# Optimization experiments

Measured on AMD Instinct MI355X. Metric: run time of the kernel, lower is better.

The kernel has to match this reference:

```python
import jax, jax.numpy as jnp
import numpy as np

N_NODES = 100000


def gcn_conv(x, W, b, src, dst, n):
    # PyG GCNConv: add self-loops, symmetric deg^-1/2 normalization,
    # transform then gather/scatter-add aggregate.
    loop = jnp.arange(n, dtype=src.dtype)
    s = jnp.concatenate([src, loop])
    d = jnp.concatenate([dst, loop])
    deg = jax.ops.segment_sum(jnp.ones_like(d, dtype=x.dtype), d, num_segments=n)
    dinv = jnp.where(deg > 0, 1.0 / jnp.sqrt(deg), 0.0)
    norm = dinv[s] * dinv[d]                      # [E+N]
    h = x @ W                                     # [N, out]
    msgs = h[s] * norm[:, None]                   # gather + scale
    out = jax.ops.segment_sum(msgs, d, num_segments=n)  # scatter-add
    return out + b


def setup_inputs() -> dict:
    key = jax.random.key(0)
    k1, k2, k3, k4 = jax.random.split(key, 4)
    F_in, H, D = 128, 16, 128
    x = jax.random.normal(k1, (N_NODES, F_in), dtype=jnp.float32)
    edge_index = jax.random.randint(k2, (2, 1600000), 0, N_NODES, dtype=jnp.int64)
    W1 = jax.random.normal(k3, (F_in, H), dtype=jnp.float32) / np.sqrt(F_in)
    b1 = jnp.zeros((H,), dtype=jnp.float32)
    W2 = jax.random.normal(k4, (H, D), dtype=jnp.float32) / np.sqrt(H)
    b2 = jnp.zeros((D,), dtype=jnp.float32)
    return {"x": x, "edge_index": edge_index, "W1": W1, "b1": b1, "W2": W2, "b2": b2}


def reference(x, edge_index, W1, b1, W2, b2):
    src, dst = edge_index[0], edge_index[1]
    n = x.shape[0]
    h = jax.nn.relu(gcn_conv(x, W1, b1, src, dst, n))
    out = jax.nn.relu(gcn_conv(h, W2, b2, src, dst, n))
    return out
```

## Files before the change

kernel.cpp:

```cpp
#include <hip/hip_runtime.h>
#include <hip/hip_fp16.h>
#include <stdint.h>

#define F_IN  128
#define HID   16
#define F_OUT 128
#define NBK   256
#define NBLK  256
#define BCAP  8192
#define LCAP  512

__device__ __forceinline__ int bucket_of(int d, int N) {
    return (int)(((long long)d * NBK) / N);
}
__device__ __forceinline__ int bucket_lo(int b, int N) {
    return (int)(((long long)b * N + NBK - 1) / NBK);
}

__global__ void k_initb(int* __restrict__ bcur) {
    bcur[threadIdx.x] = threadIdx.x * BCAP;
}

__global__ void k_partf(const int* __restrict__ ei, int* __restrict__ bcur,
                        uint32_t* __restrict__ pairs, int E, int N) {
    __shared__ int lh[NBK], lbase[NBK], lcur[NBK], lnlo[NBK];
    int blk = blockIdx.x, t = threadIdx.x;
    int C = (E + NBLK - 1) / NBLK;
    int e0 = blk * C;
    int e1 = e0 + C; if (e1 > E) e1 = E;
    for (int i = t; i < NBK; i += 256) { lh[i] = 0; lcur[i] = 0; lnlo[i] = bucket_lo(i, N); }
    __syncthreads();
    for (int e = e0 + t; e < e1; e += 256)
        atomicAdd(&lh[bucket_of(ei[E + e], N)], 1);
    __syncthreads();
    {
        int i = (t + blk) & (NBK - 1);
        lbase[i] = lh[i] ? atomicAdd(&bcur[i], lh[i]) : 0;
    }
    __syncthreads();
    for (int e = e0 + t; e < e1; e += 256) {
        int s = ei[e];
        int d = ei[E + e];
        int b = bucket_of(d, N);
        int pos = lbase[b] + atomicAdd(&lcur[b], 1);
        if (pos < (b + 1) * BCAP)
            pairs[pos] = ((uint32_t)s << 10) | (uint32_t)(d - lnlo[b]);
    }
}

__global__ void k_csr2(const uint32_t* __restrict__ pairs, const int* __restrict__ bcur,
                       int* __restrict__ row_start, int* __restrict__ cnt,
                       float* __restrict__ dinv, int* __restrict__ srcs, int N) {
    __shared__ int lcnt[LCAP];
    __shared__ int loff[LCAP];
    __shared__ int lcur[LCAP];
    int b = blockIdx.x, t = threadIdx.x;
    int base = b * BCAP;
    int ec = bcur[b] - base; if (ec > BCAP) ec = BCAP;
    int nlo = bucket_lo(b, N);
    int nhi = bucket_lo(b + 1, N); if (nhi > N) nhi = N;
    int nn = nhi - nlo;
    lcnt[t] = 0; lcnt[t + 256] = 0;
    __syncthreads();
    for (int e = t; e < ec; e += 256)
        atomicAdd(&lcnt[pairs[base + e] & 1023u], 1);
    __syncthreads();
    int v0 = lcnt[t], v1 = lcnt[t + 256];
    int p0 = (v0 + 3) & ~3, p1 = (v1 + 3) & ~3;
    loff[t] = p0; loff[t + 256] = p1;
    __syncthreads();
    for (int o = 1; o < LCAP; o <<= 1) {
        int a0 = (t >= o) ? loff[t - o] : 0;
        int a1 = (t + 256 >= o) ? loff[t + 256 - o] : 0;
        __syncthreads();
        loff[t] += a0; loff[t + 256] += a1;
        __syncthreads();
    }
    if (t < nn) {
        int gs = base + (loff[t] - p0);
        row_start[nlo + t] = gs;
        cnt[nlo + t]       = v0;
        dinv[nlo + t]      = rsqrtf((float)(v0 + 1));
        lcur[t]            = gs;
    }
    int t2 = t + 256;
    if (t2 < nn) {
        int gs = base + (loff[t2] - p1);
        row_start[nlo + t2] = gs;
        cnt[nlo + t2]       = v1;
        dinv[nlo + t2]      = rsqrtf((float)(v1 + 1));
        lcur[t2]            = gs;
    }
    __syncthreads();
    for (int e = t; e < ec; e += 256) {
        uint32_t p = pairs[base + e];
        int pos = atomicAdd(&lcur[p & 1023u], 1);
        srcs[pos] = (int)(p >> 10);
    }
}

#define XP1 132
__global__ void __launch_bounds__(256) k_transform1(
        const float* __restrict__ x, const float* __restrict__ W1,
        const float* __restrict__ dinv, __half* __restrict__ g1, int n) {
    __shared__ float sX[32 * XP1];
    __shared__ float sWt[HID * XP1];
    int t = threadIdx.x;
    int node0 = blockIdx.x * 32;
    for (int i = t; i < F_IN * HID; i += 256) {
        int k = i >> 4, f = i & 15;
        sWt[f * XP1 + k] = W1[i];
    }
    const float4* x4 = (const float4*)(x + (size_t)node0 * F_IN);
    int nrem = n - node0;
#pragma unroll
    for (int j = 0; j < 4; ++j) {
        int idx4 = t + j * 256;
        int nl = idx4 >> 5;
        int kk = (idx4 & 31) * 4;
        float4 v = make_float4(0.f, 0.f, 0.f, 0.f);
        if (nl < nrem) v = x4[idx4];
        *(float4*)&sX[nl * XP1 + kk] = v;
    }
    __syncthreads();
    int f  = t & 7;
    int nl = t >> 3;
    float a0 = 0.f, a1 = 0.f;
    const float* xr  = &sX[nl * XP1];
    const float* wr0 = &sWt[f * XP1];
    const float* wr1 = &sWt[(f + 8) * XP1];
#pragma unroll 4
    for (int k = 0; k < F_IN; k += 4) {
        float4 xv = *(const float4*)(xr + k);
        float4 w0 = *(const float4*)(wr0 + k);
        float4 w1 = *(const float4*)(wr1 + k);
        a0 += xv.x * w0.x + xv.y * w0.y + xv.z * w0.z + xv.w * w0.w;
        a1 += xv.x * w1.x + xv.y * w1.y + xv.z * w1.z + xv.w * w1.w;
    }
    int node = node0 + nl;
    if (node < n) {
        float di = dinv[node];
        g1[(size_t)node * HID + f]     = __float2half(di * a0);
        g1[(size_t)node * HID + f + 8] = __float2half(di * a1);
    }
}

__device__ __forceinline__ void add_h8(float* __restrict__ acc, const __half* __restrict__ ptr) {
    uint4 u = *(const uint4*)ptr;
    const __half2* h = (const __half2*)&u;
#pragma unroll
    for (int i = 0; i < 4; ++i) {
        float2 f = __half22float2(h[i]);
        acc[2 * i]     += f.x;
        acc[2 * i + 1] += f.y;
    }
}

template<bool EP1>
__global__ void __launch_bounds__(256) k_gather_h(
        const __half* __restrict__ g, const int* __restrict__ srcs,
        const int* __restrict__ row_start, const int* __restrict__ cnt,
        const float* __restrict__ dinv, const float* __restrict__ b1,
        __half* __restrict__ outb, int n) {
    int t = blockIdx.x * blockDim.x + threadIdx.x;
    int node = t >> 1;
    int p = t & 1;
    if (node >= n) return;
    int rs  = row_start[node];
    int deg = cnt[node];
    float acc[8];
    {
        uint4 u = *(const uint4*)(g + (size_t)node * HID + p * 8);
        const __half2* h = (const __half2*)&u;
#pragma unroll
        for (int i = 0; i < 4; ++i) {
            float2 f = __half22float2(h[i]);
            acc[2 * i] = f.x; acc[2 * i + 1] = f.y;
        }
    }
    int j = 0;
    for (; j + 8 <= deg; j += 8) {
        int4 ia = *(const int4*)(srcs + rs + j);
        int4 ib = *(const int4*)(srcs + rs + j + 4);
        add_h8(acc, g + (size_t)ia.x * HID + p * 8);
        add_h8(acc, g + (size_t)ia.y * HID + p * 8);
        add_h8(acc, g + (size_t)ia.z * HID + p * 8);
        add_h8(acc, g + (size_t)ia.w * HID + p * 8);
        add_h8(acc, g + (size_t)ib.x * HID + p * 8);
        add_h8(acc, g + (size_t)ib.y * HID + p * 8);
        add_h8(acc, g + (size_t)ib.z * HID + p * 8);
        add_h8(acc, g + (size_t)ib.w * HID + p * 8);
    }
    if (j + 4 <= deg) {
        int4 ia = *(const int4*)(srcs + rs + j);
        add_h8(acc, g + (size_t)ia.x * HID + p * 8);
        add_h8(acc, g + (size_t)ia.y * HID + p * 8);
        add_h8(acc, g + (size_t)ia.z * HID + p * 8);
        add_h8(acc, g + (size_t)ia.w * HID + p * 8);
        j += 4;
    }
    for (; j < deg; ++j)
        add_h8(acc, g + (size_t)srcs[rs + j] * HID + p * 8);
    if (EP1) {
        float di = dinv[node];
#pragma unroll
        for (int i = 0; i < 8; ++i)
            acc[i] = di * fmaxf(di * acc[i] + b1[p * 8 + i], 0.0f);
    }
    uint4 o;
    __half2* oh = (__half2*)&o;
#pragma unroll
    for (int i = 0; i < 4; ++i)
        oh[i] = __floats2half2_rn(acc[2 * i], acc[2 * i + 1]);
    *(uint4*)(outb + (size_t)node * HID + p * 8) = o;
}

__global__ void __launch_bounds__(256) k_transform2(
        const __half* __restrict__ agg, const float* __restrict__ W2,
        const float* __restrict__ b2, const float* __restrict__ dinv,
        float* __restrict__ out, int n) {
    int t = threadIdx.x;
    int d = t & 127;
    int h = t >> 7;
    int node0 = blockIdx.x * 32;
    float wcol[HID];
#pragma unroll
    for (int f = 0; f < HID; ++f) wcol[f] = W2[f * F_OUT + d];
    float bd = b2[d];
#pragma unroll 4
    for (int i = 0; i < 16; ++i) {
        int node = node0 + h + 2 * i;
        if (node >= n) continue;
        const uint4* av = (const uint4*)(agg + (size_t)node * HID);
        uint4 u0 = av[0], u1 = av[1];
        const __half2* h0 = (const __half2*)&u0;
        const __half2* h1 = (const __half2*)&u1;
        float s = 0.f;
#pragma unroll
        for (int q = 0; q < 4; ++q) {
            float2 f0 = __half22float2(h0[q]);
            float2 f1 = __half22float2(h1[q]);
            s += f0.x * wcol[2 * q]     + f0.y * wcol[2 * q + 1];
            s += f1.x * wcol[8 + 2 * q] + f1.y * wcol[9 + 2 * q];
        }
        out[(size_t)node * F_OUT + d] = fmaxf(dinv[node] * s + bd, 0.0f);
    }
}

extern "C" void kernel_launch(void* const* d_in, const int* in_sizes, int n_in,
                              void* d_out, int out_size, void* d_ws, size_t ws_size,
                              hipStream_t stream) {
    const float* x  = (const float*)d_in[0];
    const int*   ei = (const int*)d_in[1];
    const float* W1 = (const float*)d_in[2];
    const float* b1 = (const float*)d_in[3];
    const float* W2 = (const float*)d_in[4];
    const float* b2 = (const float*)d_in[5];
    float* out = (float*)d_out;

    const int N = in_sizes[0] / F_IN;
    const int E = in_sizes[1] / 2;

    float* dinv      = (float*)d_ws;
    int*   cnt       = (int*)(dinv + N);
    int*   row_start = cnt + N;
    int*   bcur      = row_start + N;
    int*   srcs      = bcur + NBK;
    uintptr_t xb = (uintptr_t)(srcs + (size_t)NBK * BCAP + 64);
    xb = (xb + 15) & ~(uintptr_t)15;
    uint32_t* pairs = (uint32_t*)xb;
    __half* bufA = (__half*)xb;
    __half* bufB = bufA + (size_t)N * HID;

    k_initb<<<1, NBK, 0, stream>>>(bcur);
    k_partf<<<NBLK, 256, 0, stream>>>(ei, bcur, pairs, E, N);
    k_csr2 <<<NBK, 256, 0, stream>>>(pairs, bcur, row_start, cnt, dinv, srcs, N);

    k_transform1<<<(N + 31) / 32, 256, 0, stream>>>(x, W1, dinv, bufA, N);
    k_gather_h<true> <<<((size_t)N * 2 + 255) / 256, 256, 0, stream>>>(
        bufA, srcs, row_start, cnt, dinv, b1, bufB, N);
    k_gather_h<false><<<((size_t)N * 2 + 255) / 256, 256, 0, stream>>>(
        bufB, srcs, row_start, cnt, dinv, b1, bufA, N);
    k_transform2<<<(N + 31) / 32, 256, 0, stream>>>(bufA, W2, b2, dinv, out, N);
}
```

Measured before the change: 218.7 us.

## Double CSR buckets and split gather across four threads per node

Doubles the destination buckets to 512 with half the per-bucket capacity. The CSR build now runs 512 blocks, each covering at most 256 nodes with a single-element scan per thread. The gather kernels use four threads per node, each handling 4 half features with 8-byte loads, instead of two threads with 16-byte loads. This raises parallelism and cuts per-thread register and latency chains. The bucket-cursor init kernel becomes a memset, with bucket bases added in the partition kernel. The trade-off is smaller vector loads, more index reads per node, and a tighter bucket capacity margin.

```diff
diff --git a/kernel.cpp b/kernel.cpp
--- a/kernel.cpp
+++ b/kernel.cpp
@@ -5,20 +5,15 @@
 #define F_IN  128
 #define HID   16
 #define F_OUT 128
-#define NBK   256
+#define NBK   512
 #define NBLK  256
-#define BCAP  8192
-#define LCAP  512
+#define BCAP  4096
 
 __device__ __forceinline__ int bucket_of(int d, int N) {
     return (int)(((long long)d * NBK) / N);
 }
 __device__ __forceinline__ int bucket_lo(int b, int N) {
     return (int)(((long long)b * N + NBK - 1) / NBK);
-}
-
-__global__ void k_initb(int* __restrict__ bcur) {
-    bcur[threadIdx.x] = threadIdx.x * BCAP;
 }
 
 __global__ void k_partf(const int* __restrict__ ei, int* __restrict__ bcur,
@@ -33,9 +28,9 @@
     for (int e = e0 + t; e < e1; e += 256)
         atomicAdd(&lh[bucket_of(ei[E + e], N)], 1);
     __syncthreads();
-    {
-        int i = (t + blk) & (NBK - 1);
-        lbase[i] = lh[i] ? atomicAdd(&bcur[i], lh[i]) : 0;
+    for (int w = 0; w < NBK; w += 256) {
+        int i = (t + w + blk) & (NBK - 1);
+        lbase[i] = i * BCAP + (lh[i] ? atomicAdd(&bcur[i], lh[i]) : 0);
     }
     __syncthreads();
     for (int e = e0 + t; e < e1; e += 256) {
@@ -48,48 +43,40 @@
     }
 }
 
-__global__ void k_csr2(const uint32_t* __restrict__ pairs, const int* __restrict__ bcur,
-                       int* __restrict__ row_start, int* __restrict__ cnt,
-                       float* __restrict__ dinv, int* __restrict__ srcs, int N) {
-    __shared__ int lcnt[LCAP];
-    __shared__ int loff[LCAP];
-    __shared__ int lcur[LCAP];
+__global__ void __launch_bounds__(256) k_csr2(
+        const uint32_t* __restrict__ pairs, const int* __restrict__ bcur,
+        int* __restrict__ row_start, int* __restrict__ cnt,
+        float* __restrict__ dinv, int* __restrict__ srcs, int N) {
+    __shared__ int lcnt[256];
+    __shared__ int loff[256];
+    __shared__ int lcur[256];
     int b = blockIdx.x, t = threadIdx.x;
     int base = b * BCAP;
-    int ec = bcur[b] - base; if (ec > BCAP) ec = BCAP;
+    int ec = bcur[b]; if (ec > BCAP) ec = BCAP;
     int nlo = bucket_lo(b, N);
     int nhi = bucket_lo(b + 1, N); if (nhi > N) nhi = N;
     int nn = nhi - nlo;
-    lcnt[t] = 0; lcnt[t + 256] = 0;
+    lcnt[t] = 0;
     __syncthreads();
     for (int e = t; e < ec; e += 256)
         atomicAdd(&lcnt[pairs[base + e] & 1023u], 1);
     __syncthreads();
-    int v0 = lcnt[t], v1 = lcnt[t + 256];
-    int p0 = (v0 + 3) & ~3, p1 = (v1 + 3) & ~3;
-    loff[t] = p0; loff[t + 256] = p1;
-    __syncthreads();
-    for (int o = 1; o < LCAP; o <<= 1) {
-        int a0 = (t >= o) ? loff[t - o] : 0;
-        int a1 = (t + 256 >= o) ? loff[t + 256 - o] : 0;
+    int v = lcnt[t];
+    int pv = (v + 3) & ~3;
+    loff[t] = pv;
+    __syncthreads();
+    for (int o = 1; o < 256; o <<= 1) {
+        int a = (t >= o) ? loff[t - o] : 0;
         __syncthreads();
-        loff[t] += a0; loff[t + 256] += a1;
+        loff[t] += a;
         __syncthreads();
     }
     if (t < nn) {
-        int gs = base + (loff[t] - p0);
+        int gs = base + (loff[t] - pv);
         row_start[nlo + t] = gs;
-        cnt[nlo + t]       = v0;
-        dinv[nlo + t]      = rsqrtf((float)(v0 + 1));
+        cnt[nlo + t]       = v;
+        dinv[nlo + t]      = rsqrtf((float)(v + 1));
         lcur[t]            = gs;
-    }
-    int t2 = t + 256;
-    if (t2 < nn) {
-        int gs = base + (loff[t2] - p1);
-        row_start[nlo + t2] = gs;
-        cnt[nlo + t2]       = v1;
-        dinv[nlo + t2]      = rsqrtf((float)(v1 + 1));
-        lcur[t2]            = gs;
     }
     __syncthreads();
     for (int e = t; e < ec; e += 256) {
@@ -145,15 +132,12 @@
     }
 }
 
-__device__ __forceinline__ void add_h8(float* __restrict__ acc, const __half* __restrict__ ptr) {
-    uint4 u = *(const uint4*)ptr;
+__device__ __forceinline__ void add_h4(float* __restrict__ acc, const __half* __restrict__ ptr) {
+    uint2 u = *(const uint2*)ptr;
     const __half2* h = (const __half2*)&u;
-#pragma unroll
-    for (int i = 0; i < 4; ++i) {
-        float2 f = __half22float2(h[i]);
-        acc[2 * i]     += f.x;
-        acc[2 * i + 1] += f.y;
-    }
+    float2 f0 = __half22float2(h[0]);
+    float2 f1 = __half22float2(h[1]);
+    acc[0] += f0.x; acc[1] += f0.y; acc[2] += f1.x; acc[3] += f1.y;
 }
 
 template<bool EP1>
@@ -163,56 +147,53 @@
         const float* __restrict__ dinv, const float* __restrict__ b1,
         __half* __restrict__ outb, int n) {
     int t = blockIdx.x * blockDim.x + threadIdx.x;
-    int node = t >> 1;
-    int p = t & 1;
+    int node = t >> 2;
+    int p = t & 3;
     if (node >= n) return;
     int rs  = row_start[node];
     int deg = cnt[node];
-    float acc[8];
+    float acc[4];
     {
-        uint4 u = *(const uint4*)(g + (size_t)node * HID + p * 8);
+        uint2 u = *(const uint2*)(g + (size_t)node * HID + p * 4);
         const __half2* h = (const __half2*)&u;
-#pragma unroll
-        for (int i = 0; i < 4; ++i) {
-            float2 f = __half22float2(h[i]);
-            acc[2 * i] = f.x; acc[2 * i + 1] = f.y;
-        }
+        float2 f0 = __half22float2(h[0]);
+        float2 f1 = __half22float2(h[1]);
+        acc[0] = f0.x; acc[1] = f0.y; acc[2] = f1.x; acc[3] = f1.y;
     }
     int j = 0;
     for (; j + 8 <= deg; j += 8) {
         int4 ia = *(const int4*)(srcs + rs + j);
         int4 ib = *(const int4*)(srcs + rs + j + 4);
-        add_h8(acc, g + (size_t)ia.x * HID + p * 8);
-        add_h8(acc, g + (size_t)ia.y * HID + p * 8);
-        add_h8(acc, g + (size_t)ia.z * HID + p * 8);
-        add_h8(acc, g + (size_t)ia.w * HID + p * 8);
-        add_h8(acc, g + (size_t)ib.x * HID + p * 8);
-        add_h8(acc, g + (size_t)ib.y * HID + p * 8);
-        add_h8(acc, g + (size_t)ib.z * HID + p * 8);
-        add_h8(acc, g + (size_t)ib.w * HID + p * 8);
+        add_h4(acc, g + (size_t)ia.x * HID + p * 4);
+        add_h4(acc, g + (size_t)ia.y * HID + p * 4);
+        add_h4(acc, g + (size_t)ia.z * HID + p * 4);
+        add_h4(acc, g + (size_t)ia.w * HID + p * 4);
+        add_h4(acc, g + (size_t)ib.x * HID + p * 4);
+        add_h4(acc, g + (size_t)ib.y * HID + p * 4);
+        add_h4(acc, g + (size_t)ib.z * HID + p * 4);
+        add_h4(acc, g + (size_t)ib.w * HID + p * 4);
     }
     if (j + 4 <= deg) {
         int4 ia = *(const int4*)(srcs + rs + j);
-        add_h8(acc, g + (size_t)ia.x * HID + p * 8);
-        add_h8(acc, g + (size_t)ia.y * HID + p * 8);
-        add_h8(acc, g + (size_t)ia.z * HID + p * 8);
-        add_h8(acc, g + (size_t)ia.w * HID + p * 8);
+        add_h4(acc, g + (size_t)ia.x * HID + p * 4);
+        add_h4(acc, g + (size_t)ia.y * HID + p * 4);
+        add_h4(acc, g + (size_t)ia.z * HID + p * 4);
+        add_h4(acc, g + (size_t)ia.w * HID + p * 4);
         j += 4;
     }
     for (; j < deg; ++j)
-        add_h8(acc, g + (size_t)srcs[rs + j] * HID + p * 8);
+        add_h4(acc, g + (size_t)srcs[rs + j] * HID + p * 4);
     if (EP1) {
         float di = dinv[node];
 #pragma unroll
-        for (int i = 0; i < 8; ++i)
-            acc[i] = di * fmaxf(di * acc[i] + b1[p * 8 + i], 0.0f);
-    }
-    uint4 o;
+        for (int i = 0; i < 4; ++i)
+            acc[i] = di * fmaxf(di * acc[i] + b1[p * 4 + i], 0.0f);
+    }
+    uint2 o;
     __half2* oh = (__half2*)&o;
-#pragma unroll
-    for (int i = 0; i < 4; ++i)
-        oh[i] = __floats2half2_rn(acc[2 * i], acc[2 * i + 1]);
-    *(uint4*)(outb + (size_t)node * HID + p * 8) = o;
+    oh[0] = __floats2half2_rn(acc[0], acc[1]);
+    oh[1] = __floats2half2_rn(acc[2], acc[3]);
+    *(uint2*)(outb + (size_t)node * HID + p * 4) = o;
 }
 
 __global__ void __launch_bounds__(256) k_transform2(
@@ -272,14 +253,14 @@
     __half* bufA = (__half*)xb;
     __half* bufB = bufA + (size_t)N * HID;
 
-    k_initb<<<1, NBK, 0, stream>>>(bcur);
+    hipMemsetAsync(bcur, 0, NBK * sizeof(int), stream);
     k_partf<<<NBLK, 256, 0, stream>>>(ei, bcur, pairs, E, N);
     k_csr2 <<<NBK, 256, 0, stream>>>(pairs, bcur, row_start, cnt, dinv, srcs, N);
 
     k_transform1<<<(N + 31) / 32, 256, 0, stream>>>(x, W1, dinv, bufA, N);
-    k_gather_h<true> <<<((size_t)N * 2 + 255) / 256, 256, 0, stream>>>(
+    k_gather_h<true> <<<((size_t)N * 4 + 255) / 256, 256, 0, stream>>>(
         bufA, srcs, row_start, cnt, dinv, b1, bufB, N);
-    k_gather_h<false><<<((size_t)N * 2 + 255) / 256, 256, 0, stream>>>(
+    k_gather_h<false><<<((size_t)N * 4 + 255) / 256, 256, 0, stream>>>(
         bufB, srcs, row_start, cnt, dinv, b1, bufA, N);
     k_transform2<<<(N + 31) / 32, 256, 0, stream>>>(bufA, W2, b2, dinv, out, N);
 }
```

New measurement: 212.9 us. 2.7% less time.
